# Optimization experiments

Hardware: AMD Instinct MI355X
Metric: run time of the kernel (lower is better)

Reference implementation:

```python
import jax, jax.numpy as jnp
import numpy as np
from jax import lax

H_LSTM = 2048

def setup_inputs() -> dict:
    key = jax.random.key(0)
    ks = jax.random.split(key, 8)
    N, T = 32, 20
    inp = {
        'base_out': jax.random.normal(ks[0], (N * T, 12, 4096), jnp.float32) * 0.1,
        'dist': jax.random.uniform(ks[1], (N, T, 2, 2, 12, 12), jnp.float32),
        'W1': jax.random.normal(ks[2], (4096, 4096), jnp.float32) * 0.02,
        'W2': jax.random.normal(ks[3], (2048, 2048), jnp.float32) * 0.02,
        'w_ih': jax.random.normal(ks[4], (4 * H_LSTM, 3072), jnp.float32) * 0.02,
        'w_hh': jax.random.normal(ks[5], (4 * H_LSTM, H_LSTM), jnp.float32) * 0.02,
        'b_ih': jnp.zeros((4 * H_LSTM,), jnp.float32),
        'b_hh': jnp.zeros((4 * H_LSTM,), jnp.float32),
        'Wc': jax.random.normal(ks[6], (8, H_LSTM), jnp.float32) * 0.01,
        'bc': jnp.zeros((8,), jnp.float32),
        'N': N,
        'T': T,
    }
    return inp

def _lstm(x, w_ih, w_hh, b_ih, b_hh):
    # x: [seq, batch, in]; torch gate order i, f, g, o
    seq, batch, _ = x.shape
    h0 = jnp.zeros((batch, H_LSTM), x.dtype)
    def step(carry, xt):
        h, c = carry
        gates = xt @ w_ih.T + b_ih + h @ w_hh.T + b_hh
        i, f, g, o = jnp.split(gates, 4, axis=-1)
        c = jax.nn.sigmoid(f) * c + jax.nn.sigmoid(i) * jnp.tanh(g)
        h = jax.nn.sigmoid(o) * jnp.tanh(c)
        return (h, c), h
    (_, _), hs = lax.scan(step, (h0, h0), x)
    return hs  # [seq, batch, H]

def reference(base_out, dist, W1, W2, w_ih, w_hh, b_ih, b_hh, Wc, bc, N, T):
    NT = N * T
    distb = dist[:, :, 1].reshape(NT, 2, 12, 12)
    distc = dist[:, :, 0].reshape(NT, 2, 12, 12)
    # conv1da: 1x1 conv == per-node linear; base_out [NT,12,4096] -> [NT,4096,12]
    node1 = jnp.einsum('oc,nvc->nov', W1, base_out).reshape(NT, 2, 2048, 12)
    n1 = jnp.einsum('nkcv,nkvw->ncw', node1, distb) + jnp.einsum('nkcv,nkvw->ncw', node1, distc)
    node1 = jax.nn.relu(n1)  # [NT,2048,12]
    node2 = jnp.einsum('oc,ncv->nov', W2, node1).reshape(NT, 2, 1024, 12)
    n2b = jax.nn.relu(jnp.einsum('nkcv,nkvw->ncw', node2, distb))  # [NT,1024,12]
    n2c = jax.nn.relu(jnp.einsum('nkcv,nkvw->ncw', node2, distc))
    left = n2b[:, :, :6].mean(axis=2)
    right = n2b[:, :, 6:].mean(axis=2)
    allf = n2c.mean(axis=2)
    pooled = jnp.concatenate([left, right, allf], axis=1).reshape(N, T, 3072)
    # torch nn.LSTM default is seq-first: sequence dim = N, batch dim = T (faithful)
    video_feat = _lstm(pooled, w_ih, w_hh, b_ih, b_hh)  # [N, T, 2048]
    group_cls = video_feat[:, -1, :] @ Wc.T + bc  # [N, num_classes]
    return group_cls, video_feat
```

## Files before the change

### kernel.cpp

```cpp
#include <hip/hip_runtime.h>

typedef _Float16 f16x8 __attribute__((ext_vector_type(8)));
typedef _Float16 f16x4 __attribute__((ext_vector_type(4)));
typedef __attribute__((ext_vector_type(4))) float f32x4;
typedef __attribute__((ext_vector_type(4))) unsigned int u32x4;

#define DI __device__ __forceinline__

DI void gload16(const void* g, void* l) {
  __builtin_amdgcn_global_load_lds(
      (const __attribute__((address_space(1))) unsigned int*)g,
      (__attribute__((address_space(3))) unsigned int*)l, 16, 0, 0);
}

DI float sigm(float x) { return 1.f / (1.f + __expf(-x)); }
DI float tanh_(float x) { return 2.f / (1.f + __expf(-2.f * x)) - 1.f; }

__global__ __launch_bounds__(256) void cvt4h(const float* __restrict__ in,
                                             _Float16* __restrict__ out, int n4) {
  int i = blockIdx.x * 256 + threadIdx.x;
  if (i >= n4) return;
  float4 v = ((const float4*)in)[i];
  f16x4 o;
  o[0] = (_Float16)v.x; o[1] = (_Float16)v.y; o[2] = (_Float16)v.z; o[3] = (_Float16)v.w;
  ((f16x4*)out)[i] = o;
}

__global__ __launch_bounds__(512, 2)
void gemm256(const _Float16* __restrict__ A, const _Float16* __restrict__ B,
             _Float16* __restrict__ C, int M, int N, int K) {
  extern __shared__ _Float16 sm[];
  _Float16* smA = sm;
  _Float16* smB = sm + 32768;

  const int t512 = threadIdx.x;
  const int lane = t512 & 63, wid = t512 >> 6;
  const int wm = (wid >> 2) * 128, wn = (wid & 3) * 64;
  const int lr = lane & 15, lg = lane >> 4;
  const int sg0 = lg ^ (lr & 7), sg1 = (4 + lg) ^ (lr & 7);

  const int nwgx = gridDim.x;
  int id = blockIdx.y * nwgx + blockIdx.x;
  int nwg = nwgx * gridDim.y;
  if ((nwg & 7) == 0) id = (id & 7) * (nwg >> 3) + (id >> 3);
  const int n0 = (id % nwgx) * 256;
  const int m0 = (id / nwgx) * 256;

  f32x4 acc[8][4] = {};

#define STAGE(kt, buf)                                                         \
  {                                                                            \
    const int kbase = (kt) * 64;                                               \
    _Pragma("unroll") for (int i = 0; i < 4; ++i) {                            \
      int G = t512 + i * 512;                                                  \
      int r = G >> 3, gs = (G & 7) ^ (r & 7);                                  \
      gload16(A + (size_t)(m0 + r) * K + kbase + gs * 8,                       \
              smA + (buf) * 16384 + G * 8);                                    \
    }                                                                          \
    _Pragma("unroll") for (int i = 0; i < 4; ++i) {                            \
      int G = t512 + i * 512;                                                  \
      int r = G >> 3, gs = (G & 7) ^ (r & 7);                                  \
      gload16(B + (size_t)(n0 + r) * K + kbase + gs * 8,                       \
              smB + (buf) * 16384 + G * 8);                                    \
    }                                                                          \
  }

#define PHASE(m0f, n0f)                                                        \
  {                                                                            \
    f16x8 av[4][2], bv[2][2];                                                  \
    _Pragma("unroll") for (int im = 0; im < 4; ++im) {                         \
      int row = wm + (m0f + im) * 16 + lr;                                     \
      av[im][0] = *(const f16x8*)(Ab + row * 128 + sg0 * 16);                  \
      av[im][1] = *(const f16x8*)(Ab + row * 128 + sg1 * 16);                  \
    }                                                                          \
    _Pragma("unroll") for (int jn = 0; jn < 2; ++jn) {                         \
      int row = wn + (n0f + jn) * 16 + lr;                                     \
      bv[jn][0] = *(const f16x8*)(Bb + row * 128 + sg0 * 16);                  \
      bv[jn][1] = *(const f16x8*)(Bb + row * 128 + sg1 * 16);                  \
    }                                                                          \
    _Pragma("unroll") for (int im = 0; im < 4; ++im)                           \
        _Pragma("unroll") for (int jn = 0; jn < 2; ++jn) {                     \
      acc[m0f + im][n0f + jn] = __builtin_amdgcn_mfma_f32_16x16x32_f16(        \
          av[im][0], bv[jn][0], acc[m0f + im][n0f + jn], 0, 0, 0);             \
      acc[m0f + im][n0f + jn] = __builtin_amdgcn_mfma_f32_16x16x32_f16(        \
          av[im][1], bv[jn][1], acc[m0f + im][n0f + jn], 0, 0, 0);             \
    }                                                                          \
  }

  STAGE(0, 0);
  const int NT = K >> 6;
  for (int t = 0; t < NT; ++t) {
    const int c = t & 1;
    if (t + 1 < NT) {
      STAGE(t + 1, c ^ 1);
      asm volatile("s_waitcnt vmcnt(8)" ::: "memory");
    } else {
      asm volatile("s_waitcnt vmcnt(0)" ::: "memory");
    }
    __builtin_amdgcn_s_barrier();
    __builtin_amdgcn_sched_barrier(0);
    const char* Ab = (const char*)(smA + c * 16384);
    const char* Bb = (const char*)(smB + c * 16384);
    PHASE(0, 0)
    PHASE(0, 2)
    PHASE(4, 0)
    PHASE(4, 2)
    __builtin_amdgcn_s_barrier();
    __builtin_amdgcn_sched_barrier(0);
  }
#undef STAGE
#undef PHASE

#pragma unroll
  for (int m = 0; m < 8; ++m)
#pragma unroll
    for (int n = 0; n < 4; ++n)
#pragma unroll
      for (int q = 0; q < 4; ++q) {
        int row = m0 + wm + m * 16 + lg * 4 + q;
        int col = n0 + wn + n * 16 + lr;
        C[(size_t)row * N + col] = (_Float16)acc[m][n][q];
      }
}

template <int OUTMODE>
__global__ __launch_bounds__(256, 2)
void gemm_bt(const _Float16* __restrict__ A, const _Float16* __restrict__ B,
             void* __restrict__ Cout, const float* __restrict__ bias1,
             const float* __restrict__ bias2, int M, int N, int K) {
  __shared__ alignas(16) _Float16 Asm[128 * 32];
  __shared__ alignas(16) _Float16 Bsm[128 * 32];
  const int t = threadIdx.x;
  const int lane = t & 63, wid = t >> 6;
  const int m0 = blockIdx.y * 128, n0 = blockIdx.x * 128;
  const int wm = (wid >> 1) * 64, wn = (wid & 1) * 64;
  const int lr = lane & 15, lk = (lane >> 4) * 8, lg = lane >> 4;

  f32x4 acc[4][4] = {};

  const int e0 = t, e1 = t + 256;
  const int ra0 = e0 >> 2, ka0 = (e0 & 3) << 3;
  const int ra1 = e1 >> 2, ka1 = (e1 & 3) << 3;

  for (int kt = 0; kt < K; kt += 32) {
    gload16(A + (size_t)(m0 + ra0) * K + kt + ka0, &Asm[e0 * 8]);
    gload16(A + (size_t)(m0 + ra1) * K + kt + ka1, &Asm[e1 * 8]);
    gload16(B + (size_t)(n0 + ra0) * K + kt + ka0, &Bsm[e0 * 8]);
    gload16(B + (size_t)(n0 + ra1) * K + kt + ka1, &Bsm[e1 * 8]);
    __syncthreads();
    f16x8 af[4], bfr[4];
#pragma unroll
    for (int f = 0; f < 4; ++f) {
      af[f] = *(const f16x8*)&Asm[(wm + f * 16 + lr) * 32 + lk];
      bfr[f] = *(const f16x8*)&Bsm[(wn + f * 16 + lr) * 32 + lk];
    }
#pragma unroll
    for (int i = 0; i < 4; ++i)
#pragma unroll
      for (int j = 0; j < 4; ++j)
        acc[i][j] = __builtin_amdgcn_mfma_f32_16x16x32_f16(af[i], bfr[j], acc[i][j], 0, 0, 0);
    __syncthreads();
  }

#pragma unroll
  for (int i = 0; i < 4; ++i) {
#pragma unroll
    for (int j = 0; j < 4; ++j) {
#pragma unroll
      for (int q = 0; q < 4; ++q) {
        int row = m0 + wm + i * 16 + lg * 4 + q;
        int col = n0 + wn + j * 16 + lr;
        if constexpr (OUTMODE == 0) {
          ((_Float16*)Cout)[(size_t)row * N + col] = (_Float16)acc[i][j][q];
        } else {
          ((float*)Cout)[(size_t)row * N + col] = acc[i][j][q] + bias1[col] + bias2[col];
        }
      }
    }
  }
}

__global__ __launch_bounds__(256) void mix1(const _Float16* __restrict__ node1,
                                            const float* __restrict__ dist,
                                            _Float16* __restrict__ n1t) {
  __shared__ float ds[288];
  const int nt = blockIdx.x, tid = threadIdx.x;
  for (int i = tid; i < 288; i += 256)
    ds[i] = dist[(size_t)nt * 576 + 288 + i] + dist[(size_t)nt * 576 + i];
  __syncthreads();
  const int c = blockIdx.y * 256 + tid;
  float s[12];
#pragma unroll
  for (int w = 0; w < 12; ++w) s[w] = 0.f;
#pragma unroll
  for (int k = 0; k < 2; ++k)
#pragma unroll
    for (int v = 0; v < 12; ++v) {
      float x = (float)node1[(size_t)(nt * 12 + v) * 4096 + k * 2048 + c];
      const float* d = &ds[k * 144 + v * 12];
#pragma unroll
      for (int w = 0; w < 12; ++w) s[w] = fmaf(x, d[w], s[w]);
    }
#pragma unroll
  for (int w = 0; w < 12; ++w)
    n1t[(size_t)(nt * 12 + w) * 2048 + c] = (_Float16)fmaxf(s[w], 0.f);
}

__global__ __launch_bounds__(256) void mix2(const _Float16* __restrict__ node2,
                                            const float* __restrict__ dist,
                                            _Float16* __restrict__ pooled) {
  __shared__ float db[288], dc[288];
  const int nt = blockIdx.x, tid = threadIdx.x;
  for (int i = tid; i < 288; i += 256) {
    db[i] = dist[(size_t)nt * 576 + 288 + i];
    dc[i] = dist[(size_t)nt * 576 + i];
  }
  __syncthreads();
  const int c = blockIdx.y * 256 + tid;
  float sb[12], sc[12];
#pragma unroll
  for (int w = 0; w < 12; ++w) { sb[w] = 0.f; sc[w] = 0.f; }
#pragma unroll
  for (int k = 0; k < 2; ++k)
#pragma unroll
    for (int v = 0; v < 12; ++v) {
      float x = (float)node2[(size_t)(nt * 12 + v) * 2048 + k * 1024 + c];
      const float* pb = &db[k * 144 + v * 12];
      const float* pc = &dc[k * 144 + v * 12];
#pragma unroll
      for (int w = 0; w < 12; ++w) { sb[w] = fmaf(x, pb[w], sb[w]); sc[w] = fmaf(x, pc[w], sc[w]); }
    }
  float left = 0.f, right = 0.f, allf = 0.f;
#pragma unroll
  for (int w = 0; w < 6; ++w) left += fmaxf(sb[w], 0.f);
#pragma unroll
  for (int w = 6; w < 12; ++w) right += fmaxf(sb[w], 0.f);
#pragma unroll
  for (int w = 0; w < 12; ++w) allf += fmaxf(sc[w], 0.f);
  pooled[(size_t)nt * 3072 + c] = (_Float16)(left * (1.f / 6.f));
  pooled[(size_t)nt * 3072 + 1024 + c] = (_Float16)(right * (1.f / 6.f));
  pooled[(size_t)nt * 3072 + 2048 + c] = (_Float16)(allf * (1.f / 12.f));
}

__global__ __launch_bounds__(256, 1) void lstm_persist3(
    const _Float16* __restrict__ whh,
    const float* __restrict__ xg,
    _Float16* __restrict__ hbuf,
    float* __restrict__ vf,
    int* __restrict__ go,
    int* __restrict__ flags) {
  extern __shared__ char lds[];
  char* hls = lds;
  char* wls = lds + 81920;
  float* Y = (float*)(lds + 147456);
  const int tid = threadIdx.x, bid = blockIdx.x, cb = bid * 8;
  const int lane = tid & 63, wid = tid >> 6;
  const int mi = wid >> 1, ni = wid & 1;
  const int lr = lane & 15, lg = lane >> 4;
  const int n = ni * 16 + lr;
  const _Float16* wp = whh + (size_t)((n >> 3) * 2048 + cb + (n & 7)) * 2048;
  const int arow = mi * 16 + lr;
  const int arow_c = (arow < 20) ? arow : (16 + (lr & 3));
  const int axor = arow_c & 7;
  const int pt = tid >> 3, pj = tid & 7;
  float c_reg = 0.f;

  for (int i = tid; i < 4096; i += 256) {
    int r = i >> 8, gg = i & 255;
    u32x4 v = *(const u32x4*)(whh + (size_t)((r >> 3) * 2048 + cb + (r & 7)) * 2048 + gg * 8);
    *(u32x4*)(wls + (((r) << 8) + (gg ^ (r & 7))) * 16) = v;
  }

  for (int s = 0; s < 32; ++s) {
    if (s > 0) {
      const _Float16* hsrc = hbuf + ((s - 1) & 1) * 65536;
      u32x4 tmp[20];
#pragma unroll
      for (int j = 0; j < 20; ++j) {
        asm volatile("global_load_dwordx4 %0, %1, off sc0 sc1"
                     : "=v"(tmp[j]) : "v"(hsrc + j * 2048 + tid * 8));
      }
      asm volatile("s_waitcnt vmcnt(0)" ::: "memory");
      __builtin_amdgcn_sched_barrier(0);
#pragma unroll
      for (int j = 0; j < 20; ++j)
        *(u32x4*)(hls + (((j) << 8) + (tid ^ (j & 7))) * 16) = tmp[j];
      __syncthreads();
      f32x4 acc = {};
      if (ni == 0) {
#pragma unroll 8
        for (int kt = 0; kt < 2048; kt += 32) {
          int g = (kt >> 3) + lg;
          f16x8 a = *(const f16x8*)(hls + ((arow_c << 8) + (g ^ axor)) * 16);
          f16x8 w = *(const f16x8*)(wls + ((n << 8) + (g ^ (n & 7))) * 16);
          acc = __builtin_amdgcn_mfma_f32_16x16x32_f16(a, w, acc, 0, 0, 0);
        }
      } else {
#pragma unroll 8
        for (int kt = 0; kt < 2048; kt += 32) {
          int g = (kt >> 3) + lg;
          f16x8 a = *(const f16x8*)(hls + ((arow_c << 8) + (g ^ axor)) * 16);
          f16x8 w = *(const f16x8*)(wp + kt + lg * 8);
          acc = __builtin_amdgcn_mfma_f32_16x16x32_f16(a, w, acc, 0, 0, 0);
        }
      }
#pragma unroll
      for (int q = 0; q < 4; ++q) {
        int t = mi * 16 + lg * 4 + q;
        if (t < 20) Y[t * 32 + n] = acc[q];
      }
    }
    __syncthreads();
    if (tid < 160) {
      float g0 = xg[(size_t)(s * 20 + pt) * 8192 + cb + pj];
      float g1 = xg[(size_t)(s * 20 + pt) * 8192 + 2048 + cb + pj];
      float g2 = xg[(size_t)(s * 20 + pt) * 8192 + 4096 + cb + pj];
      float g3 = xg[(size_t)(s * 20 + pt) * 8192 + 6144 + cb + pj];
      if (s > 0) {
        g0 += Y[pt * 32 + pj];
        g1 += Y[pt * 32 + 8 + pj];
        g2 += Y[pt * 32 + 16 + pj];
        g3 += Y[pt * 32 + 24 + pj];
      }
      float cn = sigm(g1) * c_reg + sigm(g0) * tanh_(g2);
      float hv = sigm(g3) * tanh_(cn);
      c_reg = cn;
      union { _Float16 f; unsigned short u; } cv;
      cv.f = (_Float16)hv;
      int mine = cv.u;
      int oth = __shfl_xor(mine, 1, 64);
      if ((tid & 1) == 0) {
        unsigned int packed = ((unsigned)mine & 0xffffu) | ((unsigned)oth << 16);
        __hip_atomic_store((unsigned int*)(hbuf + (s & 1) * 65536 + pt * 2048 + cb + pj),
                           packed, __ATOMIC_RELAXED, __HIP_MEMORY_SCOPE_AGENT);
      }
      vf[(size_t)(s * 20 + pt) * 2048 + cb + pj] = hv;
    }
    if (s == 31) break;
    asm volatile("s_waitcnt vmcnt(0)" ::: "memory");
    __syncthreads();
    if (bid == 0) {
      if (tid > 0) {
        while (__hip_atomic_load(&flags[tid * 16], __ATOMIC_RELAXED,
                                 __HIP_MEMORY_SCOPE_AGENT) < s + 1)
          __builtin_amdgcn_s_sleep(2);
      }
      __syncthreads();
      if (tid < 8)
        __hip_atomic_store(&go[tid * 16], s + 1, __ATOMIC_RELAXED,
                           __HIP_MEMORY_SCOPE_AGENT);
    } else {
      if (tid == 0) {
        __hip_atomic_store(&flags[bid * 16], s + 1, __ATOMIC_RELAXED,
                           __HIP_MEMORY_SCOPE_AGENT);
        while (__hip_atomic_load(&go[(bid & 7) * 16], __ATOMIC_RELAXED,
                                 __HIP_MEMORY_SCOPE_AGENT) < s + 1)
          __builtin_amdgcn_s_sleep(4);
      }
      __syncthreads();
    }
  }
}

__global__ __launch_bounds__(256) void gcls(const float* __restrict__ vf,
                                            const float* __restrict__ Wc,
                                            const float* __restrict__ bc,
                                            float* __restrict__ out) {
  const int n = blockIdx.x;
  const int j = threadIdx.x >> 5, l = threadIdx.x & 31;
  const float* v = vf + (size_t)(n * 20 + 19) * 2048;
  const float* w = Wc + (size_t)j * 2048;
  float s = 0.f;
  for (int c = l; c < 2048; c += 32) s += v[c] * w[c];
  for (int off = 16; off > 0; off >>= 1) s += __shfl_down(s, off, 32);
  if (l == 0) out[n * 8 + j] = s + bc[j];
}

extern "C" void kernel_launch(void* const* d_in, const int* in_sizes, int n_in,
                              void* d_out, int out_size, void* d_ws, size_t ws_size,
                              hipStream_t stream) {
  const float* base_out = (const float*)d_in[0];
  const float* dist = (const float*)d_in[1];
  const float* W1 = (const float*)d_in[2];
  const float* W2 = (const float*)d_in[3];
  const float* w_ih = (const float*)d_in[4];
  const float* w_hh = (const float*)d_in[5];
  const float* b_ih = (const float*)d_in[6];
  const float* b_hh = (const float*)d_in[7];
  const float* Wc = (const float*)d_in[8];
  const float* bc = (const float*)d_in[9];
  float* out = (float*)d_out;

  char* ws = (char*)d_ws;
  const size_t MB = 1048576;
  _Float16* Ahf   = (_Float16*)(ws + 0);
  _Float16* W1hf  = (_Float16*)(ws + 60 * MB);
  _Float16* node1 = (_Float16*)(ws + 92 * MB);
  _Float16* whhhf = (_Float16*)(ws + 152 * MB);
  _Float16* wihhf = (_Float16*)(ws + 184 * MB);
  float* xg       = (float*)(ws + 232 * MB);
  int* go         = (int*)(ws + 252 * MB);
  int* flags      = (int*)(ws + 252 * MB + 1024);
  _Float16* hbuf  = (_Float16*)(ws + 252 * MB + 65536);
  _Float16* W2hf  = (_Float16*)(ws + 255 * MB);
  _Float16* pooled= (_Float16*)(ws + 263 * MB);
  _Float16* n1t   = (_Float16*)(ws + 0);
  _Float16* node2 = (_Float16*)(ws + 30 * MB);

  hipFuncSetAttribute((const void*)gemm256,
                      hipFuncAttributeMaxDynamicSharedMemorySize, 131072);
  hipFuncSetAttribute((const void*)lstm_persist3,
                      hipFuncAttributeMaxDynamicSharedMemorySize, 150016);

  cvt4h<<<30720, 256, 0, stream>>>(base_out, Ahf, 7864320);
  cvt4h<<<16384, 256, 0, stream>>>(W1, W1hf, 4194304);
  cvt4h<<<4096, 256, 0, stream>>>(W2, W2hf, 1048576);
  cvt4h<<<24576, 256, 0, stream>>>(w_ih, wihhf, 6291456);
  cvt4h<<<16384, 256, 0, stream>>>(w_hh, whhhf, 4194304);

  gemm256<<<dim3(16, 30), 512, 131072, stream>>>(Ahf, W1hf, node1, 7680, 4096, 4096);
  mix1<<<dim3(640, 8), 256, 0, stream>>>(node1, dist, n1t);
  gemm256<<<dim3(8, 30), 512, 131072, stream>>>(n1t, W2hf, node2, 7680, 2048, 2048);
  mix2<<<dim3(640, 4), 256, 0, stream>>>(node2, dist, pooled);
  gemm_bt<1><<<dim3(64, 5), 256, 0, stream>>>(pooled, wihhf, xg, b_ih, b_hh,
                                              640, 8192, 3072);
  hipMemsetAsync(go, 0, 65536, stream);
  lstm_persist3<<<256, 256, 150016, stream>>>(whhhf, xg, hbuf, out + 256, go, flags);
  gcls<<<32, 256, 0, stream>>>(out + 256, Wc, bc, out);
}
```

Measured before the change: 787.4 us.

## Split LSTM h-vector load into two halves overlapped with MFMA

In the persistent LSTM kernel, each step now loads the previous hidden state in two halves along K. The second half's global loads are in flight while the MFMA loop over the first half runs. The xg input-gate loads are also hoisted to the start of each step so their latency overlaps the recurrent matmul. This shortens the serial critical path of each timestep, at the cost of an extra block barrier and more live registers per step.

Result: no change. 794.7 us (+0.9%).

```diff
diff --git a/kernel.cpp b/kernel.cpp
--- a/kernel.cpp
+++ b/kernel.cpp
@@ -242,7 +242,7 @@
   pooled[(size_t)nt * 3072 + 2048 + c] = (_Float16)(allf * (1.f / 12.f));
 }
 
-__global__ __launch_bounds__(256, 1) void lstm_persist3(
+__global__ __launch_bounds__(256, 1) void lstm_persist4(
     const _Float16* __restrict__ whh,
     const float* __restrict__ xg,
     _Float16* __restrict__ hbuf,
@@ -263,6 +263,7 @@
   const int arow_c = (arow < 20) ? arow : (16 + (lr & 3));
   const int axor = arow_c & 7;
   const int pt = tid >> 3, pj = tid & 7;
+  const int srow = tid >> 7, sg = tid & 127;
   float c_reg = 0.f;
 
   for (int i = tid; i < 4096; i += 256) {
@@ -272,38 +273,78 @@
   }
 
   for (int s = 0; s < 32; ++s) {
+    float xg0 = 0.f, xg1 = 0.f, xg2 = 0.f, xg3 = 0.f;
+    if (tid < 160) {
+      const float* xp = xg + (size_t)(s * 20 + pt) * 8192 + cb + pj;
+      xg0 = xp[0]; xg1 = xp[2048]; xg2 = xp[4096]; xg3 = xp[6144];
+    }
     if (s > 0) {
       const _Float16* hsrc = hbuf + ((s - 1) & 1) * 65536;
-      u32x4 tmp[20];
-#pragma unroll
-      for (int j = 0; j < 20; ++j) {
+      u32x4 t1[10];
+#pragma unroll
+      for (int j = 0; j < 10; ++j) {
+        int row = j * 2 + srow;
         asm volatile("global_load_dwordx4 %0, %1, off sc0 sc1"
-                     : "=v"(tmp[j]) : "v"(hsrc + j * 2048 + tid * 8));
+                     : "=v"(t1[j]) : "v"(hsrc + row * 2048 + sg * 8));
       }
       asm volatile("s_waitcnt vmcnt(0)" ::: "memory");
       __builtin_amdgcn_sched_barrier(0);
 #pragma unroll
-      for (int j = 0; j < 20; ++j)
-        *(u32x4*)(hls + (((j) << 8) + (tid ^ (j & 7))) * 16) = tmp[j];
+      for (int j = 0; j < 10; ++j) {
+        int row = j * 2 + srow;
+        *(u32x4*)(hls + (((row) << 8) + (sg ^ (row & 7))) * 16) = t1[j];
+      }
+      u32x4 t2[10];
+#pragma unroll
+      for (int j = 0; j < 10; ++j) {
+        int row = j * 2 + srow;
+        asm volatile("global_load_dwordx4 %0, %1, off sc0 sc1"
+                     : "=v"(t2[j]) : "v"(hsrc + row * 2048 + (128 + sg) * 8));
+      }
       __syncthreads();
       f32x4 acc = {};
       if (ni == 0) {
-#pragma unroll 8
-        for (int kt = 0; kt < 2048; kt += 32) {
+#pragma unroll 4
+        for (int kt = 0; kt < 1024; kt += 32) {
           int g = (kt >> 3) + lg;
           f16x8 a = *(const f16x8*)(hls + ((arow_c << 8) + (g ^ axor)) * 16);
           f16x8 w = *(const f16x8*)(wls + ((n << 8) + (g ^ (n & 7))) * 16);
           acc = __builtin_amdgcn_mfma_f32_16x16x32_f16(a, w, acc, 0, 0, 0);
         }
       } else {
-#pragma unroll 8
-        for (int kt = 0; kt < 2048; kt += 32) {
+#pragma unroll 4
+        for (int kt = 0; kt < 1024; kt += 32) {
           int g = (kt >> 3) + lg;
           f16x8 a = *(const f16x8*)(hls + ((arow_c << 8) + (g ^ axor)) * 16);
           f16x8 w = *(const f16x8*)(wp + kt + lg * 8);
           acc = __builtin_amdgcn_mfma_f32_16x16x32_f16(a, w, acc, 0, 0, 0);
         }
       }
+      asm volatile("s_waitcnt vmcnt(0)" ::: "memory");
+      __builtin_amdgcn_sched_barrier(0);
+#pragma unroll
+      for (int j = 0; j < 10; ++j) {
+        int row = j * 2 + srow;
+        *(u32x4*)(hls + (((row) << 8) + (128 + (sg ^ (row & 7)))) * 16) = t2[j];
+      }
+      __syncthreads();
+      if (ni == 0) {
+#pragma unroll 4
+        for (int kt = 1024; kt < 2048; kt += 32) {
+          int g = (kt >> 3) + lg;
+          f16x8 a = *(const f16x8*)(hls + ((arow_c << 8) + (128 + (((g & 127)) ^ axor))) * 16);
+          f16x8 w = *(const f16x8*)(wls + ((n << 8) + (g ^ (n & 7))) * 16);
+          acc = __builtin_amdgcn_mfma_f32_16x16x32_f16(a, w, acc, 0, 0, 0);
+        }
+      } else {
+#pragma unroll 4
+        for (int kt = 1024; kt < 2048; kt += 32) {
+          int g = (kt >> 3) + lg;
+          f16x8 a = *(const f16x8*)(hls + ((arow_c << 8) + (128 + (((g & 127)) ^ axor))) * 16);
+          f16x8 w = *(const f16x8*)(wp + kt + lg * 8);
+          acc = __builtin_amdgcn_mfma_f32_16x16x32_f16(a, w, acc, 0, 0, 0);
+        }
+      }
 #pragma unroll
       for (int q = 0; q < 4; ++q) {
         int t = mi * 16 + lg * 4 + q;
@@ -312,10 +353,7 @@
     }
     __syncthreads();
     if (tid < 160) {
-      float g0 = xg[(size_t)(s * 20 + pt) * 8192 + cb + pj];
-      float g1 = xg[(size_t)(s * 20 + pt) * 8192 + 2048 + cb + pj];
-      float g2 = xg[(size_t)(s * 20 + pt) * 8192 + 4096 + cb + pj];
-      float g3 = xg[(size_t)(s * 20 + pt) * 8192 + 6144 + cb + pj];
+      float g0 = xg0, g1 = xg1, g2 = xg2, g3 = xg3;
       if (s > 0) {
         g0 += Y[pt * 32 + pj];
         g1 += Y[pt * 32 + 8 + pj];
@@ -409,7 +447,7 @@
 
   hipFuncSetAttribute((const void*)gemm256,
                       hipFuncAttributeMaxDynamicSharedMemorySize, 131072);
-  hipFuncSetAttribute((const void*)lstm_persist3,
+  hipFuncSetAttribute((const void*)lstm_persist4,
                       hipFuncAttributeMaxDynamicSharedMemorySize, 150016);
 
   cvt4h<<<30720, 256, 0, stream>>>(base_out, Ahf, 7864320);
@@ -425,6 +463,6 @@
   gemm_bt<1><<<dim3(64, 5), 256, 0, stream>>>(pooled, wihhf, xg, b_ih, b_hh,
                                               640, 8192, 3072);
   hipMemsetAsync(go, 0, 65536, stream);
-  lstm_persist3<<<256, 256, 150016, stream>>>(whhhf, xg, hbuf, out + 256, go, flags);
+  lstm_persist4<<<256, 256, 150016, stream>>>(whhhf, xg, hbuf, out + 256, go, flags);
   gcls<<<32, 256, 0, stream>>>(out + 256, Wc, bc, out);
 }
```

## Halve persistent LSTM grid to 128 blocks with 16 hidden units each

Applied to the files above, without the earlier changes.

The persistent LSTM recurrence kernel now assigns 16 hidden columns per block and runs 128 blocks instead of 256. Each wave owns one gate's 16 columns and computes two MFMA tiles covering all 20 batch rows. The intent is to cut grid-barrier participants and per-block h-reload traffic per step. The cost is that each block streams more W_hh from global memory (three of four gates are not LDS-resident), so per-step latency per block may rise.

After: 862.7 us. +9.6%, slower.

```diff
diff --git a/kernel.cpp b/kernel.cpp
--- a/kernel.cpp
+++ b/kernel.cpp
@@ -242,7 +242,7 @@
   pooled[(size_t)nt * 3072 + 2048 + c] = (_Float16)(allf * (1.f / 12.f));
 }
 
-__global__ __launch_bounds__(256, 1) void lstm_persist3(
+__global__ __launch_bounds__(256, 1) void lstm_persist5(
     const _Float16* __restrict__ whh,
     const float* __restrict__ xg,
     _Float16* __restrict__ hbuf,
@@ -253,22 +253,17 @@
   char* hls = lds;
   char* wls = lds + 81920;
   float* Y = (float*)(lds + 147456);
-  const int tid = threadIdx.x, bid = blockIdx.x, cb = bid * 8;
-  const int lane = tid & 63, wid = tid >> 6;
-  const int mi = wid >> 1, ni = wid & 1;
+  const int tid = threadIdx.x, bid = blockIdx.x, cb = bid * 16;
+  const int lane = tid & 63, w = tid >> 6;
   const int lr = lane & 15, lg = lane >> 4;
-  const int n = ni * 16 + lr;
-  const _Float16* wp = whh + (size_t)((n >> 3) * 2048 + cb + (n & 7)) * 2048;
-  const int arow = mi * 16 + lr;
-  const int arow_c = (arow < 20) ? arow : (16 + (lr & 3));
-  const int axor = arow_c & 7;
-  const int pt = tid >> 3, pj = tid & 7;
-  float c_reg = 0.f;
+  const _Float16* wp = whh + (size_t)(w * 2048 + cb + lr) * 2048;
+  const int arow1 = (lr < 4) ? (16 + lr) : (16 + (lr & 3));
+  float c0 = 0.f, c1 = 0.f;
 
   for (int i = tid; i < 4096; i += 256) {
     int r = i >> 8, gg = i & 255;
-    u32x4 v = *(const u32x4*)(whh + (size_t)((r >> 3) * 2048 + cb + (r & 7)) * 2048 + gg * 8);
-    *(u32x4*)(wls + (((r) << 8) + (gg ^ (r & 7))) * 16) = v;
+    u32x4 v = *(const u32x4*)(whh + (size_t)(cb + r) * 2048 + gg * 8);
+    *(u32x4*)(wls + ((r << 8) + (gg ^ (r & 7))) * 16) = v;
   }
 
   for (int s = 0; s < 32; ++s) {
@@ -284,63 +279,72 @@
       __builtin_amdgcn_sched_barrier(0);
 #pragma unroll
       for (int j = 0; j < 20; ++j)
-        *(u32x4*)(hls + (((j) << 8) + (tid ^ (j & 7))) * 16) = tmp[j];
+        *(u32x4*)(hls + ((j << 8) + (tid ^ (j & 7))) * 16) = tmp[j];
       __syncthreads();
-      f32x4 acc = {};
-      if (ni == 0) {
+      f32x4 acc0 = {}, acc1 = {};
+      if (w == 0) {
 #pragma unroll 8
         for (int kt = 0; kt < 2048; kt += 32) {
           int g = (kt >> 3) + lg;
-          f16x8 a = *(const f16x8*)(hls + ((arow_c << 8) + (g ^ axor)) * 16);
-          f16x8 w = *(const f16x8*)(wls + ((n << 8) + (g ^ (n & 7))) * 16);
-          acc = __builtin_amdgcn_mfma_f32_16x16x32_f16(a, w, acc, 0, 0, 0);
+          f16x8 a0 = *(const f16x8*)(hls + ((lr << 8) + (g ^ (lr & 7))) * 16);
+          f16x8 a1 = *(const f16x8*)(hls + ((arow1 << 8) + (g ^ (arow1 & 7))) * 16);
+          f16x8 wv = *(const f16x8*)(wls + ((lr << 8) + (g ^ (lr & 7))) * 16);
+          acc0 = __builtin_amdgcn_mfma_f32_16x16x32_f16(a0, wv, acc0, 0, 0, 0);
+          acc1 = __builtin_amdgcn_mfma_f32_16x16x32_f16(a1, wv, acc1, 0, 0, 0);
         }
       } else {
 #pragma unroll 8
         for (int kt = 0; kt < 2048; kt += 32) {
           int g = (kt >> 3) + lg;
-          f16x8 a = *(const f16x8*)(hls + ((arow_c << 8) + (g ^ axor)) * 16);
-          f16x8 w = *(const f16x8*)(wp + kt + lg * 8);
-          acc = __builtin_amdgcn_mfma_f32_16x16x32_f16(a, w, acc, 0, 0, 0);
+          f16x8 a0 = *(const f16x8*)(hls + ((lr << 8) + (g ^ (lr & 7))) * 16);
+          f16x8 a1 = *(const f16x8*)(hls + ((arow1 << 8) + (g ^ (arow1 & 7))) * 16);
+          f16x8 wv = *(const f16x8*)(wp + kt + lg * 8);
+          acc0 = __builtin_amdgcn_mfma_f32_16x16x32_f16(a0, wv, acc0, 0, 0, 0);
+          acc1 = __builtin_amdgcn_mfma_f32_16x16x32_f16(a1, wv, acc1, 0, 0, 0);
         }
       }
 #pragma unroll
       for (int q = 0; q < 4; ++q) {
-        int t = mi * 16 + lg * 4 + q;
-        if (t < 20) Y[t * 32 + n] = acc[q];
+        int t = lg * 4 + q;
+        Y[t * 64 + w * 16 + lr] = acc0[q];
+        if (lg == 0) Y[(16 + q) * 64 + w * 16 + lr] = acc1[q];
       }
     }
     __syncthreads();
-    if (tid < 160) {
-      float g0 = xg[(size_t)(s * 20 + pt) * 8192 + cb + pj];
-      float g1 = xg[(size_t)(s * 20 + pt) * 8192 + 2048 + cb + pj];
-      float g2 = xg[(size_t)(s * 20 + pt) * 8192 + 4096 + cb + pj];
-      float g3 = xg[(size_t)(s * 20 + pt) * 8192 + 6144 + cb + pj];
-      if (s > 0) {
-        g0 += Y[pt * 32 + pj];
-        g1 += Y[pt * 32 + 8 + pj];
-        g2 += Y[pt * 32 + 16 + pj];
-        g3 += Y[pt * 32 + 24 + pj];
-      }
-      float cn = sigm(g1) * c_reg + sigm(g0) * tanh_(g2);
-      float hv = sigm(g3) * tanh_(cn);
-      c_reg = cn;
-      union { _Float16 f; unsigned short u; } cv;
-      cv.f = (_Float16)hv;
-      int mine = cv.u;
-      int oth = __shfl_xor(mine, 1, 64);
-      if ((tid & 1) == 0) {
-        unsigned int packed = ((unsigned)mine & 0xffffu) | ((unsigned)oth << 16);
-        __hip_atomic_store((unsigned int*)(hbuf + (s & 1) * 65536 + pt * 2048 + cb + pj),
-                           packed, __ATOMIC_RELAXED, __HIP_MEMORY_SCOPE_AGENT);
-      }
-      vf[(size_t)(s * 20 + pt) * 2048 + cb + pj] = hv;
+#pragma unroll
+    for (int b2 = 0; b2 < 2; ++b2) {
+      int idx = tid + b2 * 256;
+      if (idx < 320) {
+        int t = idx >> 4, j = idx & 15;
+        const float* xp = xg + (size_t)(s * 20 + t) * 8192 + cb + j;
+        float g0 = xp[0], g1 = xp[2048], g2 = xp[4096], g3 = xp[6144];
+        if (s > 0) {
+          g0 += Y[t * 64 + j];
+          g1 += Y[t * 64 + 16 + j];
+          g2 += Y[t * 64 + 32 + j];
+          g3 += Y[t * 64 + 48 + j];
+        }
+        float cp = (b2 == 0) ? c0 : c1;
+        float cn = sigm(g1) * cp + sigm(g0) * tanh_(g2);
+        float hv = sigm(g3) * tanh_(cn);
+        if (b2 == 0) c0 = cn; else c1 = cn;
+        union { _Float16 f; unsigned short u; } cv;
+        cv.f = (_Float16)hv;
+        int mine = cv.u;
+        int oth = __shfl_xor(mine, 1, 64);
+        if ((lane & 1) == 0) {
+          unsigned int packed = ((unsigned)mine & 0xffffu) | ((unsigned)oth << 16);
+          __hip_atomic_store((unsigned int*)(hbuf + (s & 1) * 65536 + t * 2048 + cb + j),
+                             packed, __ATOMIC_RELAXED, __HIP_MEMORY_SCOPE_AGENT);
+        }
+        vf[(size_t)(s * 20 + t) * 2048 + cb + j] = hv;
+      }
     }
     if (s == 31) break;
     asm volatile("s_waitcnt vmcnt(0)" ::: "memory");
     __syncthreads();
     if (bid == 0) {
-      if (tid > 0) {
+      if (tid > 0 && tid < 128) {
         while (__hip_atomic_load(&flags[tid * 16], __ATOMIC_RELAXED,
                                  __HIP_MEMORY_SCOPE_AGENT) < s + 1)
           __builtin_amdgcn_s_sleep(2);
@@ -409,8 +413,8 @@
 
   hipFuncSetAttribute((const void*)gemm256,
                       hipFuncAttributeMaxDynamicSharedMemorySize, 131072);
-  hipFuncSetAttribute((const void*)lstm_persist3,
-                      hipFuncAttributeMaxDynamicSharedMemorySize, 150016);
+  hipFuncSetAttribute((const void*)lstm_persist5,
+                      hipFuncAttributeMaxDynamicSharedMemorySize, 152576);
 
   cvt4h<<<30720, 256, 0, stream>>>(base_out, Ahf, 7864320);
   cvt4h<<<16384, 256, 0, stream>>>(W1, W1hf, 4194304);
@@ -425,6 +429,6 @@
   gemm_bt<1><<<dim3(64, 5), 256, 0, stream>>>(pooled, wihhf, xg, b_ih, b_hh,
                                               640, 8192, 3072);
   hipMemsetAsync(go, 0, 65536, stream);
-  lstm_persist3<<<256, 256, 150016, stream>>>(whhhf, xg, hbuf, out + 256, go, flags);
+  lstm_persist5<<<128, 256, 152576, stream>>>(whhhf, xg, hbuf, out + 256, go, flags);
   gcls<<<32, 256, 0, stream>>>(out + 256, Wc, bc, out);
 }
```
